# Performance work log

Hardware: AMD Instinct MI355X
Metric: run time of the kernel (lower is better)

## Reference

```python
import jax, jax.numpy as jnp
import numpy as np

E = 512   # fusion_dim
H = 8     # num_heads
HD = E // H
NC = 6

def _ln(x, g, b, eps=1e-5):
    m = jnp.mean(x, axis=-1, keepdims=True)
    v = jnp.mean((x - m) ** 2, axis=-1, keepdims=True)
    return (x - m) * jax.lax.rsqrt(v + eps) * g + b

def _lin(x, w, b):
    # torch nn.Linear: w is (out, in)
    return x @ w.T + b

def setup_inputs() -> dict:
    key = jax.random.key(0)
    ks = iter(jax.random.split(key, 32))
    B = 16384
    d = {
        'rgb':  jax.random.normal(next(ks), (B, 768), jnp.float32),
        'pose': jax.random.normal(next(ks), (B, 640), jnp.float32),
        'flow': jax.random.normal(next(ks), (B, 1024), jnp.float32),
    }
    def W(k, shape):
        return jax.random.normal(k, shape, jnp.float32) * 0.02
    # projection branches: Linear + LayerNorm
    d['rgb_w'] = W(next(ks), (E, 768));  d['rgb_b'] = jnp.zeros((E,))
    d['rgb_g'] = jnp.ones((E,));         d['rgb_beta'] = jnp.zeros((E,))
    d['pose_w'] = W(next(ks), (E, 640)); d['pose_b'] = jnp.zeros((E,))
    d['pose_g'] = jnp.ones((E,));        d['pose_beta'] = jnp.zeros((E,))
    d['flow_w'] = W(next(ks), (E, 1024)); d['flow_b'] = jnp.zeros((E,))
    d['flow_g'] = jnp.ones((E,));        d['flow_beta'] = jnp.zeros((E,))
    # MultiheadAttention packed qkv + out proj (torch layout)
    d['in_w'] = W(next(ks), (3 * E, E)); d['in_b'] = jnp.zeros((3 * E,))
    d['out_w'] = W(next(ks), (E, E));    d['out_b'] = jnp.zeros((E,))
    # gate MLP
    d['gw1'] = W(next(ks), (E, 3 * E)); d['gb1'] = jnp.zeros((E,))
    d['gw2'] = W(next(ks), (3, E));     d['gb2'] = jnp.zeros((3,))
    # classifier
    d['cw1'] = W(next(ks), (E // 2, E)); d['cb1'] = jnp.zeros((E // 2,))
    d['cg'] = jnp.ones((E // 2,));       d['cbeta'] = jnp.zeros((E // 2,))
    d['cw2'] = W(next(ks), (NC, E // 2)); d['cb2'] = jnp.zeros((NC,))
    return d

def _forward(rgb, pose, flow, rgb_w, rgb_b, rgb_g, rgb_beta,
             pose_w, pose_b, pose_g, pose_beta,
             flow_w, flow_b, flow_g, flow_beta,
             in_w, in_b, out_w, out_b,
             gw1, gb1, gw2, gb2,
             cw1, cb1, cg, cbeta, cw2, cb2):
    # per-modality projection: Linear -> LN -> ReLU (dropout = identity, eval mode)
    r = jax.nn.relu(_ln(_lin(rgb, rgb_w, rgb_b), rgb_g, rgb_beta))
    p = jax.nn.relu(_ln(_lin(pose, pose_w, pose_b), pose_g, pose_beta))
    f = jax.nn.relu(_ln(_lin(flow, flow_w, flow_b), flow_g, flow_beta))
    stacked = jnp.stack([r, p, f], axis=1)                 # (B, 3, E)
    # self-attention over the 3 modality tokens
    qkv = stacked @ in_w.T + in_b                          # (B, 3, 3E)
    q, k, v = jnp.split(qkv, 3, axis=-1)
    B = stacked.shape[0]
    q = q.reshape(B, 3, H, HD); k = k.reshape(B, 3, H, HD); v = v.reshape(B, 3, H, HD)
    scores = jnp.einsum('bqhd,bkhd->bhqk', q, k) / np.sqrt(HD).astype(np.float32)
    attn = jax.nn.softmax(scores, axis=-1)
    ctx = jnp.einsum('bhqk,bkhd->bqhd', attn, v).reshape(B, 3, E)
    attended = ctx @ out_w.T + out_b                       # (B, 3, E)
    # gating over concatenated projections
    concat = jnp.concatenate([r, p, f], axis=1)            # (B, 3E)
    gate = jax.nn.softmax(_lin(jax.nn.relu(_lin(concat, gw1, gb1)), gw2, gb2), axis=1)  # (B, 3)
    fused = jnp.einsum('bse,bs->be', attended, gate)       # (B, E)
    # classifier
    h = jax.nn.relu(_ln(_lin(fused, cw1, cb1), cg, cbeta))
    logits = _lin(h, cw2, cb2)                             # (B, NC)
    return logits, gate

def reference(rgb, pose, flow, rgb_w, rgb_b, rgb_g, rgb_beta,
              pose_w, pose_b, pose_g, pose_beta,
              flow_w, flow_b, flow_g, flow_beta,
              in_w, in_b, out_w, out_b,
              gw1, gb1, gw2, gb2,
              cw1, cb1, cg, cbeta, cw2, cb2):
    return _forward(rgb, pose, flow, rgb_w, rgb_b, rgb_g, rgb_beta,
                    pose_w, pose_b, pose_g, pose_beta,
                    flow_w, flow_b, flow_g, flow_beta,
                    in_w, in_b, out_w, out_b,
                    gw1, gb1, gw2, gb2,
                    cw1, cb1, cg, cbeta, cw2, cb2)
```

## Files before the change

### kernel.cpp

```cpp
#include <hip/hip_runtime.h>


typedef unsigned short u16;
typedef __bf16 bf16x8 __attribute__((ext_vector_type(8)));
typedef float f32x4  __attribute__((ext_vector_type(4)));
typedef unsigned short u16x8 __attribute__((ext_vector_type(8)));
typedef unsigned short u16x4 __attribute__((ext_vector_type(4)));

#define BATCH 16384

__device__ __forceinline__ u16 f2b(float f) {
  union { float f; unsigned int u; } c; c.f = f;
  unsigned int u = c.u;
  return (u16)((u + 0x7fffu + ((u >> 16) & 1u)) >> 16);
}
__device__ __forceinline__ float b2f(u16 h) {
  union { unsigned int u; float f; } c; c.u = ((unsigned int)h) << 16;
  return c.f;
}

struct CvtJobs {
  const float* s[10];
  u16* d[10];
  int n4[10];
};

__global__ __launch_bounds__(256) void cvt_multi(CvtJobs J) {
  const int stride = gridDim.x * blockDim.x;
  const int tid = blockIdx.x * blockDim.x + threadIdx.x;
  for (int ji = 0; ji < 10; ++ji) {
    const f32x4* __restrict__ s = (const f32x4*)J.s[ji];
    u16x4* __restrict__ d = (u16x4*)J.d[ji];
    const int n4 = J.n4[ji];
    for (int i = tid; i < n4; i += stride) {
      f32x4 v = s[i];
      u16x4 o;
      #pragma unroll
      for (int c = 0; c < 4; ++c) o[c] = f2b(v[c]);
      d[i] = o;
    }
  }
}

template<int EPI>
__device__ __forceinline__ void gemm_core(
    const u16* __restrict__ A, const u16* __restrict__ Bw,
    const float* __restrict__ bias, u16* __restrict__ C,
    int K, int ldc, int coff, u16* As, u16* Bs)
{
  const int t = threadIdx.x;
  const int m0 = blockIdx.y << 7;
  const int n0 = blockIdx.x << 7;
  const int wave = t >> 6, lane = t & 63;
  const int wm = wave & 1, wn = wave >> 1;
  const int lr  = lane & 15;
  const int lk8 = (lane >> 4) << 3;
  const int srow = t >> 2;
  const int scol = (t & 3) << 4;

  f32x4 acc[4][4] = {};

  const size_t rowB = (size_t)K * 2;
  const char* Ab = (const char*)A + (size_t)m0 * rowB + scol;
  const char* Bb = (const char*)Bw + (size_t)n0 * rowB + scol;

  auto stage = [&](int s, int buf) {
    const char* Ak = Ab + (size_t)s * 64;
    const char* Bk = Bb + (size_t)s * 64;
    #pragma unroll
    for (int j = 0; j < 2; ++j) {
      __builtin_amdgcn_global_load_lds(
          (const __attribute__((address_space(1))) void*)(Ak + (size_t)(j * 64 + srow) * rowB),
          (__attribute__((address_space(3))) void*)((char*)As + (buf << 13) + (j << 12) + (wave << 10)),
          16, 0, 0);
      __builtin_amdgcn_global_load_lds(
          (const __attribute__((address_space(1))) void*)(Bk + (size_t)(j * 64 + srow) * rowB),
          (__attribute__((address_space(3))) void*)((char*)Bs + (buf << 13) + (j << 12) + (wave << 10)),
          16, 0, 0);
    }
  };

  const int nsteps = K >> 5;
  stage(0, 0);
  for (int s = 0; s < nsteps; ++s) {
    const int cur = s & 1;
    __syncthreads();
    if (s + 1 < nsteps) stage(s + 1, cur ^ 1);

    const u16* Ac = As + (cur << 12);
    const u16* Bc = Bs + (cur << 12);
    bf16x8 af[4], bfr[4];
    #pragma unroll
    for (int mi = 0; mi < 4; ++mi) {
      const int r = (wm << 6) + (mi << 4) + lr;
      af[mi] = __builtin_bit_cast(bf16x8, *(const u16x8*)&Ac[r * 32 + lk8]);
    }
    #pragma unroll
    for (int ni = 0; ni < 4; ++ni) {
      const int r = (wn << 6) + (ni << 4) + lr;
      bfr[ni] = __builtin_bit_cast(bf16x8, *(const u16x8*)&Bc[r * 32 + lk8]);
    }
    #pragma unroll
    for (int mi = 0; mi < 4; ++mi)
      #pragma unroll
      for (int ni = 0; ni < 4; ++ni)
        acc[mi][ni] = __builtin_amdgcn_mfma_f32_16x16x32_bf16(
            af[mi], bfr[ni], acc[mi][ni], 0, 0, 0);
  }

  const int rquad = (lane >> 4) << 2;
  #pragma unroll
  for (int ni = 0; ni < 4; ++ni) {
    const int col = n0 + (wn << 6) + (ni << 4) + lr;
    const float bv = bias[col];
    #pragma unroll
    for (int mi = 0; mi < 4; ++mi) {
      const int rowb = m0 + (wm << 6) + (mi << 4) + rquad;
      #pragma unroll
      for (int r = 0; r < 4; ++r) {
        float v = acc[mi][ni][r] + bv;
        if (EPI == 2) v = fmaxf(v, 0.0f);
        C[(size_t)(rowb + r) * ldc + coff + col] = f2b(v);
      }
    }
  }
}

template<int EPI>
__global__ __launch_bounds__(256) void gemm128(
    const u16* __restrict__ A, const u16* __restrict__ Bw,
    const float* __restrict__ bias, u16* __restrict__ C,
    int K, int ldc, int coff)
{
  __shared__ __align__(16) u16 As[2][4096];
  __shared__ __align__(16) u16 Bs[2][4096];
  gemm_core<EPI>(A, Bw, bias, C, K, ldc, coff, &As[0][0], &Bs[0][0]);
}

struct P3 {
  const u16* A[3];
  const u16* W[3];
  const float* bias[3];
  int K[3];
  int coff[3];
  u16* C;
};
__global__ __launch_bounds__(256) void proj3_k(P3 p) {
  __shared__ __align__(16) u16 As[2][4096];
  __shared__ __align__(16) u16 Bs[2][4096];
  const int z = blockIdx.z;
  gemm_core<1>(p.A[z], p.W[z], p.bias[z], p.C, p.K[z], 1536, p.coff[z],
               &As[0][0], &Bs[0][0]);
}

__global__ __launch_bounds__(384) void ln3_k(
    const u16* __restrict__ raw, u16* __restrict__ dst,
    const float* __restrict__ g0, const float* __restrict__ b0,
    const float* __restrict__ g1, const float* __restrict__ b1,
    const float* __restrict__ g2, const float* __restrict__ b2)
{
  const int wave = threadIdx.x >> 6, lane = threadIdx.x & 63;
  const int m = wave % 3;
  const int b = blockIdx.x * 2 + wave / 3;
  const size_t off = (size_t)b * 1536 + m * 512 + lane * 8;
  u16x8 xa = *(const u16x8*)&raw[off];
  float x[8];
  float sum = 0.f, sq = 0.f;
  #pragma unroll
  for (int d = 0; d < 8; ++d) { float f = b2f(xa[d]); x[d] = f; sum += f; sq += f * f; }
  #pragma unroll
  for (int o = 32; o > 0; o >>= 1) { sum += __shfl_xor(sum, o); sq += __shfl_xor(sq, o); }
  const float mean = sum * (1.0f / 512.0f);
  const float var = sq * (1.0f / 512.0f) - mean * mean;
  const float rs = rsqrtf(var + 1e-5f);
  const float* g = (m == 0) ? g0 : (m == 1) ? g1 : g2;
  const float* bb = (m == 0) ? b0 : (m == 1) ? b1 : b2;
  u16x8 o;
  #pragma unroll
  for (int d = 0; d < 8; ++d) {
    float y = (x[d] - mean) * rs * g[lane * 8 + d] + bb[lane * 8 + d];
    o[d] = f2b(fmaxf(y, 0.0f));
  }
  *(u16x8*)&dst[off] = o;
}

template<int E>
__global__ __launch_bounds__(256) void ln_relu_k(
    const u16* __restrict__ src, u16* __restrict__ dst,
    const float* __restrict__ gg, const float* __restrict__ bb)
{
  constexpr int V = E >> 6;
  const int wave = threadIdx.x >> 6, lane = threadIdx.x & 63;
  const int row = blockIdx.x * 4 + wave;
  const u16* s = src + (size_t)row * E + lane * V;
  float x[V];
  float sum = 0.f, sq = 0.f;
  #pragma unroll
  for (int i = 0; i < V; i += 4) {
    u16x4 v = *(const u16x4*)(s + i);
    #pragma unroll
    for (int c = 0; c < 4; ++c) { float f = b2f(v[c]); x[i + c] = f; sum += f; sq += f * f; }
  }
  #pragma unroll
  for (int off = 32; off > 0; off >>= 1) {
    sum += __shfl_xor(sum, off);
    sq  += __shfl_xor(sq,  off);
  }
  const float invE = 1.0f / (float)E;
  const float m = sum * invE;
  const float var = sq * invE - m * m;
  const float rs = rsqrtf(var + 1e-5f);
  u16* d = dst + (size_t)row * E + lane * V;
  const float* g = gg + lane * V;
  const float* b = bb + lane * V;
  #pragma unroll
  for (int i = 0; i < V; i += 4) {
    u16x4 o;
    #pragma unroll
    for (int c = 0; c < 4; ++c) {
      float y = (x[i + c] - m) * rs * g[i + c] + b[i + c];
      o[c] = f2b(fmaxf(y, 0.0f));
    }
    *(u16x4*)(d + i) = o;
  }
}

__global__ __launch_bounds__(256) void attn_k(
    const u16* __restrict__ qkv, u16* __restrict__ ctx)
{
  const int gid = blockIdx.x * 256 + threadIdx.x;
  const int b = gid >> 6;
  const int h = (threadIdx.x >> 3) & 7;
  const int ld = threadIdx.x & 7;
  const size_t rb = (size_t)(3 * b) * 1536 + h * 64 + ld * 8;

  float q[3][8], k[3][8], v[3][8];
  #pragma unroll
  for (int i = 0; i < 3; ++i) {
    u16x8 qa = *(const u16x8*)&qkv[rb + (size_t)i * 1536];
    u16x8 ka = *(const u16x8*)&qkv[rb + (size_t)i * 1536 + 512];
    u16x8 va = *(const u16x8*)&qkv[rb + (size_t)i * 1536 + 1024];
    #pragma unroll
    for (int d = 0; d < 8; ++d) { q[i][d] = b2f(qa[d]); k[i][d] = b2f(ka[d]); v[i][d] = b2f(va[d]); }
  }
  float s[9];
  #pragma unroll
  for (int i = 0; i < 3; ++i)
    #pragma unroll
    for (int j = 0; j < 3; ++j) {
      float a = 0.f;
      #pragma unroll
      for (int d = 0; d < 8; ++d) a += q[i][d] * k[j][d];
      s[i * 3 + j] = a;
    }
  #pragma unroll
  for (int m = 1; m < 8; m <<= 1)
    #pragma unroll
    for (int e = 0; e < 9; ++e) s[e] += __shfl_xor(s[e], m);

  const float sc = 0.125f;
  #pragma unroll
  for (int i = 0; i < 3; ++i) {
    const float a0 = s[i * 3 + 0] * sc, a1 = s[i * 3 + 1] * sc, a2 = s[i * 3 + 2] * sc;
    const float mx = fmaxf(a0, fmaxf(a1, a2));
    float e0 = __expf(a0 - mx), e1 = __expf(a1 - mx), e2 = __expf(a2 - mx);
    const float inv = 1.0f / (e0 + e1 + e2);
    e0 *= inv; e1 *= inv; e2 *= inv;
    u16x8 o;
    #pragma unroll
    for (int d = 0; d < 8; ++d)
      o[d] = f2b(e0 * v[0][d] + e1 * v[1][d] + e2 * v[2][d]);
    *(u16x8*)&ctx[(size_t)(3 * b + i) * 512 + h * 64 + ld * 8] = o;
  }
}

__global__ __launch_bounds__(256) void gate_fuse_k(
    const u16* __restrict__ gateh, const float* __restrict__ gw2,
    const float* __restrict__ gb2, const u16* __restrict__ att,
    float* __restrict__ gate_out, u16* __restrict__ fused)
{
  const int wave = threadIdx.x >> 6, lane = threadIdx.x & 63;
  const int b = blockIdx.x * 4 + wave;
  float x[8];
  u16x8 xa = *(const u16x8*)&gateh[(size_t)b * 512 + lane * 8];
  #pragma unroll
  for (int d = 0; d < 8; ++d) x[d] = b2f(xa[d]);
  float s[3] = {0.f, 0.f, 0.f};
  #pragma unroll
  for (int j = 0; j < 3; ++j) {
    const float* w = gw2 + j * 512 + lane * 8;
    #pragma unroll
    for (int d = 0; d < 8; ++d) s[j] += x[d] * w[d];
  }
  #pragma unroll
  for (int m = 1; m < 64; m <<= 1)
    #pragma unroll
    for (int j = 0; j < 3; ++j) s[j] += __shfl_xor(s[j], m);
  #pragma unroll
  for (int j = 0; j < 3; ++j) s[j] += gb2[j];
  const float mx = fmaxf(s[0], fmaxf(s[1], s[2]));
  float g0 = __expf(s[0] - mx), g1 = __expf(s[1] - mx), g2 = __expf(s[2] - mx);
  const float inv = 1.0f / (g0 + g1 + g2);
  g0 *= inv; g1 *= inv; g2 *= inv;
  if (lane == 0) { gate_out[b * 3 + 0] = g0; gate_out[b * 3 + 1] = g1; gate_out[b * 3 + 2] = g2; }
  float o[8] = {};
  const float gw[3] = {g0, g1, g2};
  #pragma unroll
  for (int j = 0; j < 3; ++j) {
    u16x8 aa = *(const u16x8*)&att[(size_t)(3 * b + j) * 512 + lane * 8];
    #pragma unroll
    for (int d = 0; d < 8; ++d) o[d] += gw[j] * b2f(aa[d]);
  }
  u16x8 ov;
  #pragma unroll
  for (int d = 0; d < 8; ++d) ov[d] = f2b(o[d]);
  *(u16x8*)&fused[(size_t)b * 512 + lane * 8] = ov;
}

__global__ __launch_bounds__(256) void cls2_k(
    const u16* __restrict__ hh, const float* __restrict__ cw2,
    const float* __restrict__ cb2, float* __restrict__ logits)
{
  const int wave = threadIdx.x >> 6, lane = threadIdx.x & 63;
  const int b = blockIdx.x * 4 + wave;
  float x[4];
  u16x4 xa = *(const u16x4*)&hh[(size_t)b * 256 + lane * 4];
  #pragma unroll
  for (int d = 0; d < 4; ++d) x[d] = b2f(xa[d]);
  float s[6] = {};
  #pragma unroll
  for (int j = 0; j < 6; ++j) {
    const float* w = cw2 + j * 256 + lane * 4;
    #pragma unroll
    for (int d = 0; d < 4; ++d) s[j] += x[d] * w[d];
  }
  #pragma unroll
  for (int m = 1; m < 64; m <<= 1)
    #pragma unroll
    for (int j = 0; j < 6; ++j) s[j] += __shfl_xor(s[j], m);
  if (lane < 6) logits[(size_t)b * 6 + lane] = s[lane] + cb2[lane];
}

extern "C" void kernel_launch(void* const* d_in, const int* in_sizes, int n_in,
                              void* d_out, int out_size, void* d_ws, size_t ws_size,
                              hipStream_t stream) {
  const float* rgb       = (const float*)d_in[0];
  const float* pose      = (const float*)d_in[1];
  const float* flow      = (const float*)d_in[2];
  const float* rgb_w     = (const float*)d_in[3];
  const float* rgb_b     = (const float*)d_in[4];
  const float* rgb_g     = (const float*)d_in[5];
  const float* rgb_beta  = (const float*)d_in[6];
  const float* pose_w    = (const float*)d_in[7];
  const float* pose_b    = (const float*)d_in[8];
  const float* pose_g    = (const float*)d_in[9];
  const float* pose_beta = (const float*)d_in[10];
  const float* flow_w    = (const float*)d_in[11];
  const float* flow_b    = (const float*)d_in[12];
  const float* flow_g    = (const float*)d_in[13];
  const float* flow_beta = (const float*)d_in[14];
  const float* in_w      = (const float*)d_in[15];
  const float* in_b      = (const float*)d_in[16];
  const float* out_w     = (const float*)d_in[17];
  const float* out_b     = (const float*)d_in[18];
  const float* gw1       = (const float*)d_in[19];
  const float* gb1       = (const float*)d_in[20];
  const float* gw2       = (const float*)d_in[21];
  const float* gb2       = (const float*)d_in[22];
  const float* cw1       = (const float*)d_in[23];
  const float* cb1       = (const float*)d_in[24];
  const float* cg        = (const float*)d_in[25];
  const float* cbeta     = (const float*)d_in[26];
  const float* cw2       = (const float*)d_in[27];
  const float* cb2       = (const float*)d_in[28];

  float* logits_out = (float*)d_out;
  float* gate_out   = (float*)d_out + (size_t)BATCH * 6;

  char* ws = (char*)d_ws;
  u16* w_rgb  = (u16*)(ws + 0);
  u16* w_pose = (u16*)(ws + 786432);
  u16* w_flow = (u16*)(ws + 1441792);
  u16* w_in   = (u16*)(ws + 2490368);
  u16* w_out  = (u16*)(ws + 4063232);
  u16* w_g1   = (u16*)(ws + 4587520);
  u16* w_c1   = (u16*)(ws + 6160384);
  char* rpfB = ws + 6422528;
  char* ctxB = ws + 56754176;
  char* r1B  = ws + 107085824;

  u16*   rpf      = (u16*)rpfB;
  u16*   att      = (u16*)rpfB;
  u16*   raw      = (u16*)ctxB;
  u16*   ctx      = (u16*)ctxB;
  u16*   cls_tmp  = (u16*)ctxB;
  u16*   h_bf     = (u16*)(ctxB + 8388608);
  u16*   rgb_bf   = (u16*)r1B;
  u16*   pose_bf  = (u16*)(r1B + 25165824);
  u16*   flow_bf  = (u16*)(r1B + 46137344);
  u16*   qkv_buf  = (u16*)r1B;
  u16*   gateh    = (u16*)r1B;
  u16*   fusedb   = (u16*)(r1B + 16777216);

  CvtJobs J;
  const float* srcs[10] = {rgb, pose, flow, rgb_w, pose_w, flow_w, in_w, out_w, gw1, cw1};
  u16* dsts[10] = {rgb_bf, pose_bf, flow_bf, w_rgb, w_pose, w_flow, w_in, w_out, w_g1, w_c1};
  int ns[10] = {BATCH * 768, BATCH * 640, BATCH * 1024, 512 * 768, 512 * 640,
                512 * 1024, 1536 * 512, 512 * 512, 512 * 1536, 256 * 512};
  for (int i = 0; i < 10; ++i) { J.s[i] = srcs[i]; J.d[i] = dsts[i]; J.n4[i] = ns[i] / 4; }
  cvt_multi<<<2048, 256, 0, stream>>>(J);

  dim3 blk(256);
  P3 p;
  p.A[0] = rgb_bf;  p.W[0] = w_rgb;  p.bias[0] = rgb_b;  p.K[0] = 768;  p.coff[0] = 0;
  p.A[1] = pose_bf; p.W[1] = w_pose; p.bias[1] = pose_b; p.K[1] = 640;  p.coff[1] = 512;
  p.A[2] = flow_bf; p.W[2] = w_flow; p.bias[2] = flow_b; p.K[2] = 1024; p.coff[2] = 1024;
  p.C = raw;
  proj3_k<<<dim3(4, BATCH / 128, 3), blk, 0, stream>>>(p);
  ln3_k<<<BATCH / 2, dim3(384), 0, stream>>>(raw, rpf, rgb_g, rgb_beta, pose_g, pose_beta, flow_g, flow_beta);

  for (int c = 0; c < 2; ++c) {
    const u16* a_chunk = rpf + (size_t)c * 8192 * 1536;
    u16* ctx_chunk = ctx + (size_t)c * 8192 * 3 * 512;
    gemm128<1><<<dim3(12, 3 * 8192 / 128), blk, 0, stream>>>(
        a_chunk, w_in, in_b, qkv_buf, 512, 1536, 0);
    attn_k<<<8192 / 4, blk, 0, stream>>>(qkv_buf, ctx_chunk);
  }

  gemm128<2><<<dim3(4, BATCH / 128), blk, 0, stream>>>(rpf, w_g1, gb1, gateh, 1536, 512, 0);

  gemm128<1><<<dim3(4, 3 * BATCH / 128), blk, 0, stream>>>(ctx, w_out, out_b, att, 512, 512, 0);

  gate_fuse_k<<<BATCH / 4, blk, 0, stream>>>(gateh, gw2, gb2, att, gate_out, fusedb);

  gemm128<1><<<dim3(2, BATCH / 128), blk, 0, stream>>>(fusedb, w_c1, cb1, cls_tmp, 512, 256, 0);
  ln_relu_k<256><<<BATCH / 4, blk, 0, stream>>>(cls_tmp, h_bf, cg, cbeta);
  cls2_k<<<BATCH / 4, blk, 0, stream>>>(h_bf, cw2, cb2, logits_out);

  (void)in_sizes; (void)n_in; (void)out_size; (void)ws_size;
}
```

Baseline: 585.2 us.

## Fuse input fp32-to-bf16 conversion into projection GEMM and gate before out-proj

The projection GEMM now reads fp32 activations directly, converting them in registers before writing to LDS, which removes the separate conversion pass and its bf16 copy of the large inputs. The gate is computed before attention, and the attention kernel outputs the gate-weighted sum of per-modality contexts. The out-projection then runs on B rows instead of 3B. This relies on the gate summing to one so the bias is preserved, and it gives up async global-to-LDS loads for the A operand.

```diff
diff --git a/kernel.cpp b/kernel.cpp
--- a/kernel.cpp
+++ b/kernel.cpp
@@ -20,15 +20,15 @@
 }
 
 struct CvtJobs {
-  const float* s[10];
-  u16* d[10];
-  int n4[10];
+  const float* s[7];
+  u16* d[7];
+  int n4[7];
 };
 
-__global__ __launch_bounds__(256) void cvt_multi(CvtJobs J) {
+__global__ __launch_bounds__(256) void cvt_w(CvtJobs J) {
   const int stride = gridDim.x * blockDim.x;
   const int tid = blockIdx.x * blockDim.x + threadIdx.x;
-  for (int ji = 0; ji < 10; ++ji) {
+  for (int ji = 0; ji < 7; ++ji) {
     const f32x4* __restrict__ s = (const f32x4*)J.s[ji];
     u16x4* __restrict__ d = (u16x4*)J.d[ji];
     const int n4 = J.n4[ji];
@@ -43,11 +43,13 @@
 }
 
 template<int EPI>
-__device__ __forceinline__ void gemm_core(
+__global__ __launch_bounds__(256) void gemm128(
     const u16* __restrict__ A, const u16* __restrict__ Bw,
     const float* __restrict__ bias, u16* __restrict__ C,
-    int K, int ldc, int coff, u16* As, u16* Bs)
+    int K, int ldc, int coff)
 {
+  __shared__ __align__(16) u16 As[2][4096];
+  __shared__ __align__(16) u16 Bs[2][4096];
   const int t = threadIdx.x;
   const int m0 = blockIdx.y << 7;
   const int n0 = blockIdx.x << 7;
@@ -71,11 +73,11 @@
     for (int j = 0; j < 2; ++j) {
       __builtin_amdgcn_global_load_lds(
           (const __attribute__((address_space(1))) void*)(Ak + (size_t)(j * 64 + srow) * rowB),
-          (__attribute__((address_space(3))) void*)((char*)As + (buf << 13) + (j << 12) + (wave << 10)),
+          (__attribute__((address_space(3))) void*)((char*)As[buf] + (j << 12) + (wave << 10)),
           16, 0, 0);
       __builtin_amdgcn_global_load_lds(
           (const __attribute__((address_space(1))) void*)(Bk + (size_t)(j * 64 + srow) * rowB),
-          (__attribute__((address_space(3))) void*)((char*)Bs + (buf << 13) + (j << 12) + (wave << 10)),
+          (__attribute__((address_space(3))) void*)((char*)Bs[buf] + (j << 12) + (wave << 10)),
           16, 0, 0);
     }
   };
@@ -87,18 +89,16 @@
     __syncthreads();
     if (s + 1 < nsteps) stage(s + 1, cur ^ 1);
 
-    const u16* Ac = As + (cur << 12);
-    const u16* Bc = Bs + (cur << 12);
     bf16x8 af[4], bfr[4];
     #pragma unroll
     for (int mi = 0; mi < 4; ++mi) {
       const int r = (wm << 6) + (mi << 4) + lr;
-      af[mi] = __builtin_bit_cast(bf16x8, *(const u16x8*)&Ac[r * 32 + lk8]);
+      af[mi] = __builtin_bit_cast(bf16x8, *(const u16x8*)&As[cur][r * 32 + lk8]);
     }
     #pragma unroll
     for (int ni = 0; ni < 4; ++ni) {
       const int r = (wn << 6) + (ni << 4) + lr;
-      bfr[ni] = __builtin_bit_cast(bf16x8, *(const u16x8*)&Bc[r * 32 + lk8]);
+      bfr[ni] = __builtin_bit_cast(bf16x8, *(const u16x8*)&Bs[cur][r * 32 + lk8]);
     }
     #pragma unroll
     for (int mi = 0; mi < 4; ++mi)
@@ -126,31 +126,112 @@
   }
 }
 
-template<int EPI>
-__global__ __launch_bounds__(256) void gemm128(
-    const u16* __restrict__ A, const u16* __restrict__ Bw,
-    const float* __restrict__ bias, u16* __restrict__ C,
-    int K, int ldc, int coff)
-{
-  __shared__ __align__(16) u16 As[2][4096];
-  __shared__ __align__(16) u16 Bs[2][4096];
-  gemm_core<EPI>(A, Bw, bias, C, K, ldc, coff, &As[0][0], &Bs[0][0]);
-}
-
 struct P3 {
-  const u16* A[3];
+  const float* A[3];
   const u16* W[3];
   const float* bias[3];
   int K[3];
   int coff[3];
   u16* C;
 };
+
 __global__ __launch_bounds__(256) void proj3_k(P3 p) {
   __shared__ __align__(16) u16 As[2][4096];
   __shared__ __align__(16) u16 Bs[2][4096];
   const int z = blockIdx.z;
-  gemm_core<1>(p.A[z], p.W[z], p.bias[z], p.C, p.K[z], 1536, p.coff[z],
-               &As[0][0], &Bs[0][0]);
+  const float* __restrict__ A = p.A[z];
+  const u16* __restrict__ Bw = p.W[z];
+  const int K = p.K[z];
+
+  const int t = threadIdx.x;
+  const int m0 = blockIdx.y << 7;
+  const int n0 = blockIdx.x << 7;
+  const int wave = t >> 6, lane = t & 63;
+  const int wm = wave & 1, wn = wave >> 1;
+  const int lr  = lane & 15;
+  const int lk8 = (lane >> 4) << 3;
+  const int ar = t >> 3;
+  const int ac = (t & 7) << 2;
+  const int srow = t >> 2;
+  const int scol = (t & 3) << 4;
+
+  f32x4 acc[4][4] = {};
+
+  const size_t rowA = (size_t)K;
+  const size_t rowB = (size_t)K * 2;
+  const float* Abase = A + (size_t)m0 * rowA + ac;
+  const char* Bb = (const char*)Bw + (size_t)n0 * rowB + scol;
+
+  f32x4 areg[4];
+  auto loadA = [&](int s) {
+    const float* Ak = Abase + s * 32;
+    #pragma unroll
+    for (int j = 0; j < 4; ++j)
+      areg[j] = *(const f32x4*)(Ak + (size_t)(j * 32 + ar) * rowA);
+  };
+  auto writeA = [&](int buf) {
+    #pragma unroll
+    for (int j = 0; j < 4; ++j) {
+      u16x4 o;
+      #pragma unroll
+      for (int c = 0; c < 4; ++c) o[c] = f2b(areg[j][c]);
+      *(u16x4*)&As[buf][(j * 32 + ar) * 32 + ac] = o;
+    }
+  };
+  auto stageB = [&](int s, int buf) {
+    const char* Bk = Bb + (size_t)s * 64;
+    #pragma unroll
+    for (int j = 0; j < 2; ++j)
+      __builtin_amdgcn_global_load_lds(
+          (const __attribute__((address_space(1))) void*)(Bk + (size_t)(j * 64 + srow) * rowB),
+          (__attribute__((address_space(3))) void*)((char*)Bs[buf] + (j << 12) + (wave << 10)),
+          16, 0, 0);
+  };
+
+  const int nsteps = K >> 5;
+  loadA(0);
+  stageB(0, 0);
+  writeA(0);
+  for (int s = 0; s < nsteps; ++s) {
+    const int cur = s & 1;
+    __syncthreads();
+    if (s + 1 < nsteps) { loadA(s + 1); stageB(s + 1, cur ^ 1); }
+
+    bf16x8 af[4], bfr[4];
+    #pragma unroll
+    for (int mi = 0; mi < 4; ++mi) {
+      const int r = (wm << 6) + (mi << 4) + lr;
+      af[mi] = __builtin_bit_cast(bf16x8, *(const u16x8*)&As[cur][r * 32 + lk8]);
+    }
+    #pragma unroll
+    for (int ni = 0; ni < 4; ++ni) {
+      const int r = (wn << 6) + (ni << 4) + lr;
+      bfr[ni] = __builtin_bit_cast(bf16x8, *(const u16x8*)&Bs[cur][r * 32 + lk8]);
+    }
+    #pragma unroll
+    for (int mi = 0; mi < 4; ++mi)
+      #pragma unroll
+      for (int ni = 0; ni < 4; ++ni)
+        acc[mi][ni] = __builtin_amdgcn_mfma_f32_16x16x32_bf16(
+            af[mi], bfr[ni], acc[mi][ni], 0, 0, 0);
+
+    if (s + 1 < nsteps) writeA(cur ^ 1);
+  }
+
+  const int rquad = (lane >> 4) << 2;
+  #pragma unroll
+  for (int ni = 0; ni < 4; ++ni) {
+    const int col = n0 + (wn << 6) + (ni << 4) + lr;
+    const float bv = p.bias[z][col];
+    #pragma unroll
+    for (int mi = 0; mi < 4; ++mi) {
+      const int rowb = m0 + (wm << 6) + (mi << 4) + rquad;
+      #pragma unroll
+      for (int r = 0; r < 4; ++r) {
+        p.C[(size_t)(rowb + r) * 1536 + p.coff[z] + col] = f2b(acc[mi][ni][r] + bv);
+      }
+    }
+  }
 }
 
 __global__ __launch_bounds__(384) void ln3_k(
@@ -225,8 +306,42 @@
   }
 }
 
-__global__ __launch_bounds__(256) void attn_k(
-    const u16* __restrict__ qkv, u16* __restrict__ ctx)
+__global__ __launch_bounds__(256) void gate2_k(
+    const u16* __restrict__ gateh, const float* __restrict__ gw2,
+    const float* __restrict__ gb2, float* __restrict__ gate_out)
+{
+  const int wave = threadIdx.x >> 6, lane = threadIdx.x & 63;
+  const int b = blockIdx.x * 4 + wave;
+  float x[8];
+  u16x8 xa = *(const u16x8*)&gateh[(size_t)b * 512 + lane * 8];
+  #pragma unroll
+  for (int d = 0; d < 8; ++d) x[d] = b2f(xa[d]);
+  float s[3] = {0.f, 0.f, 0.f};
+  #pragma unroll
+  for (int j = 0; j < 3; ++j) {
+    const float* w = gw2 + j * 512 + lane * 8;
+    #pragma unroll
+    for (int d = 0; d < 8; ++d) s[j] += x[d] * w[d];
+  }
+  #pragma unroll
+  for (int m = 1; m < 64; m <<= 1)
+    #pragma unroll
+    for (int j = 0; j < 3; ++j) s[j] += __shfl_xor(s[j], m);
+  if (lane == 0) {
+    #pragma unroll
+    for (int j = 0; j < 3; ++j) s[j] += gb2[j];
+    const float mx = fmaxf(s[0], fmaxf(s[1], s[2]));
+    float e0 = __expf(s[0] - mx), e1 = __expf(s[1] - mx), e2 = __expf(s[2] - mx);
+    const float inv = 1.0f / (e0 + e1 + e2);
+    gate_out[b * 3 + 0] = e0 * inv;
+    gate_out[b * 3 + 1] = e1 * inv;
+    gate_out[b * 3 + 2] = e2 * inv;
+  }
+}
+
+__global__ __launch_bounds__(256) void attn_gate_k(
+    const u16* __restrict__ qkv, const float* __restrict__ gate,
+    u16* __restrict__ ctxg, int b0)
 {
   const int gid = blockIdx.x * 256 + threadIdx.x;
   const int b = gid >> 6;
@@ -258,63 +373,28 @@
     #pragma unroll
     for (int e = 0; e < 9; ++e) s[e] += __shfl_xor(s[e], m);
 
+  const float g0 = gate[(size_t)(b0 + b) * 3 + 0];
+  const float g1 = gate[(size_t)(b0 + b) * 3 + 1];
+  const float g2 = gate[(size_t)(b0 + b) * 3 + 2];
+  const float gg[3] = {g0, g1, g2};
+
+  float o[8] = {};
   const float sc = 0.125f;
   #pragma unroll
   for (int i = 0; i < 3; ++i) {
     const float a0 = s[i * 3 + 0] * sc, a1 = s[i * 3 + 1] * sc, a2 = s[i * 3 + 2] * sc;
     const float mx = fmaxf(a0, fmaxf(a1, a2));
     float e0 = __expf(a0 - mx), e1 = __expf(a1 - mx), e2 = __expf(a2 - mx);
-    const float inv = 1.0f / (e0 + e1 + e2);
+    const float inv = gg[i] / (e0 + e1 + e2);
     e0 *= inv; e1 *= inv; e2 *= inv;
-    u16x8 o;
     #pragma unroll
     for (int d = 0; d < 8; ++d)
-      o[d] = f2b(e0 * v[0][d] + e1 * v[1][d] + e2 * v[2][d]);
-    *(u16x8*)&ctx[(size_t)(3 * b + i) * 512 + h * 64 + ld * 8] = o;
-  }
-}
-
-__global__ __launch_bounds__(256) void gate_fuse_k(
-    const u16* __restrict__ gateh, const float* __restrict__ gw2,
-    const float* __restrict__ gb2, const u16* __restrict__ att,
-    float* __restrict__ gate_out, u16* __restrict__ fused)
-{
-  const int wave = threadIdx.x >> 6, lane = threadIdx.x & 63;
-  const int b = blockIdx.x * 4 + wave;
-  float x[8];
-  u16x8 xa = *(const u16x8*)&gateh[(size_t)b * 512 + lane * 8];
-  #pragma unroll
-  for (int d = 0; d < 8; ++d) x[d] = b2f(xa[d]);
-  float s[3] = {0.f, 0.f, 0.f};
-  #pragma unroll
-  for (int j = 0; j < 3; ++j) {
-    const float* w = gw2 + j * 512 + lane * 8;
-    #pragma unroll
-    for (int d = 0; d < 8; ++d) s[j] += x[d] * w[d];
-  }
-  #pragma unroll
-  for (int m = 1; m < 64; m <<= 1)
-    #pragma unroll
-    for (int j = 0; j < 3; ++j) s[j] += __shfl_xor(s[j], m);
-  #pragma unroll
-  for (int j = 0; j < 3; ++j) s[j] += gb2[j];
-  const float mx = fmaxf(s[0], fmaxf(s[1], s[2]));
-  float g0 = __expf(s[0] - mx), g1 = __expf(s[1] - mx), g2 = __expf(s[2] - mx);
-  const float inv = 1.0f / (g0 + g1 + g2);
-  g0 *= inv; g1 *= inv; g2 *= inv;
-  if (lane == 0) { gate_out[b * 3 + 0] = g0; gate_out[b * 3 + 1] = g1; gate_out[b * 3 + 2] = g2; }
-  float o[8] = {};
-  const float gw[3] = {g0, g1, g2};
-  #pragma unroll
-  for (int j = 0; j < 3; ++j) {
-    u16x8 aa = *(const u16x8*)&att[(size_t)(3 * b + j) * 512 + lane * 8];
-    #pragma unroll
-    for (int d = 0; d < 8; ++d) o[d] += gw[j] * b2f(aa[d]);
+      o[d] += e0 * v[0][d] + e1 * v[1][d] + e2 * v[2][d];
   }
   u16x8 ov;
   #pragma unroll
   for (int d = 0; d < 8; ++d) ov[d] = f2b(o[d]);
-  *(u16x8*)&fused[(size_t)b * 512 + lane * 8] = ov;
+  *(u16x8*)&ctxg[(size_t)(b0 + b) * 512 + h * 64 + ld * 8] = ov;
 }
 
 __global__ __launch_bounds__(256) void cls2_k(
@@ -386,52 +466,46 @@
   u16* w_g1   = (u16*)(ws + 4587520);
   u16* w_c1   = (u16*)(ws + 6160384);
   char* rpfB = ws + 6422528;
-  char* ctxB = ws + 56754176;
-  char* r1B  = ws + 107085824;
+  char* B2   = ws + 56754176;
+  char* Cb   = ws + 132251648;
+  char* Db   = ws + 149028864;
 
   u16*   rpf      = (u16*)rpfB;
-  u16*   att      = (u16*)rpfB;
-  u16*   raw      = (u16*)ctxB;
-  u16*   ctx      = (u16*)ctxB;
-  u16*   cls_tmp  = (u16*)ctxB;
-  u16*   h_bf     = (u16*)(ctxB + 8388608);
-  u16*   rgb_bf   = (u16*)r1B;
-  u16*   pose_bf  = (u16*)(r1B + 25165824);
-  u16*   flow_bf  = (u16*)(r1B + 46137344);
-  u16*   qkv_buf  = (u16*)r1B;
-  u16*   gateh    = (u16*)r1B;
-  u16*   fusedb   = (u16*)(r1B + 16777216);
+  u16*   raw      = (u16*)B2;
+  u16*   qkv_buf  = (u16*)B2;
+  u16*   gateh    = (u16*)Cb;
+  u16*   fusedb   = (u16*)Cb;
+  u16*   ctxg     = (u16*)Db;
+  u16*   cls_tmp  = (u16*)Db;
+  u16*   h_bf     = (u16*)(Db + 8388608);
 
   CvtJobs J;
-  const float* srcs[10] = {rgb, pose, flow, rgb_w, pose_w, flow_w, in_w, out_w, gw1, cw1};
-  u16* dsts[10] = {rgb_bf, pose_bf, flow_bf, w_rgb, w_pose, w_flow, w_in, w_out, w_g1, w_c1};
-  int ns[10] = {BATCH * 768, BATCH * 640, BATCH * 1024, 512 * 768, 512 * 640,
-                512 * 1024, 1536 * 512, 512 * 512, 512 * 1536, 256 * 512};
-  for (int i = 0; i < 10; ++i) { J.s[i] = srcs[i]; J.d[i] = dsts[i]; J.n4[i] = ns[i] / 4; }
-  cvt_multi<<<2048, 256, 0, stream>>>(J);
+  const float* srcs[7] = {rgb_w, pose_w, flow_w, in_w, out_w, gw1, cw1};
+  u16* dsts[7] = {w_rgb, w_pose, w_flow, w_in, w_out, w_g1, w_c1};
+  int ns[7] = {512 * 768, 512 * 640, 512 * 1024, 1536 * 512, 512 * 512, 512 * 1536, 256 * 512};
+  for (int i = 0; i < 7; ++i) { J.s[i] = srcs[i]; J.d[i] = dsts[i]; J.n4[i] = ns[i] / 4; }
+  cvt_w<<<128, 256, 0, stream>>>(J);
 
   dim3 blk(256);
   P3 p;
-  p.A[0] = rgb_bf;  p.W[0] = w_rgb;  p.bias[0] = rgb_b;  p.K[0] = 768;  p.coff[0] = 0;
-  p.A[1] = pose_bf; p.W[1] = w_pose; p.bias[1] = pose_b; p.K[1] = 640;  p.coff[1] = 512;
-  p.A[2] = flow_bf; p.W[2] = w_flow; p.bias[2] = flow_b; p.K[2] = 1024; p.coff[2] = 1024;
+  p.A[0] = rgb;  p.W[0] = w_rgb;  p.bias[0] = rgb_b;  p.K[0] = 768;  p.coff[0] = 0;
+  p.A[1] = pose; p.W[1] = w_pose; p.bias[1] = pose_b; p.K[1] = 640;  p.coff[1] = 512;
+  p.A[2] = flow; p.W[2] = w_flow; p.bias[2] = flow_b; p.K[2] = 1024; p.coff[2] = 1024;
   p.C = raw;
   proj3_k<<<dim3(4, BATCH / 128, 3), blk, 0, stream>>>(p);
   ln3_k<<<BATCH / 2, dim3(384), 0, stream>>>(raw, rpf, rgb_g, rgb_beta, pose_g, pose_beta, flow_g, flow_beta);
 
+  gemm128<2><<<dim3(4, BATCH / 128), blk, 0, stream>>>(rpf, w_g1, gb1, gateh, 1536, 512, 0);
+  gate2_k<<<BATCH / 4, blk, 0, stream>>>(gateh, gw2, gb2, gate_out);
+
   for (int c = 0; c < 2; ++c) {
     const u16* a_chunk = rpf + (size_t)c * 8192 * 1536;
-    u16* ctx_chunk = ctx + (size_t)c * 8192 * 3 * 512;
     gemm128<1><<<dim3(12, 3 * 8192 / 128), blk, 0, stream>>>(
         a_chunk, w_in, in_b, qkv_buf, 512, 1536, 0);
-    attn_k<<<8192 / 4, blk, 0, stream>>>(qkv_buf, ctx_chunk);
-  }
-
-  gemm128<2><<<dim3(4, BATCH / 128), blk, 0, stream>>>(rpf, w_g1, gb1, gateh, 1536, 512, 0);
-
-  gemm128<1><<<dim3(4, 3 * BATCH / 128), blk, 0, stream>>>(ctx, w_out, out_b, att, 512, 512, 0);
-
-  gate_fuse_k<<<BATCH / 4, blk, 0, stream>>>(gateh, gw2, gb2, att, gate_out, fusedb);
+    attn_gate_k<<<8192 / 4, blk, 0, stream>>>(qkv_buf, gate_out, ctxg, c * 8192);
+  }
+
+  gemm128<1><<<dim3(4, BATCH / 128), blk, 0, stream>>>(ctxg, w_out, out_b, fusedb, 512, 512, 0);
 
   gemm128<1><<<dim3(2, BATCH / 128), blk, 0, stream>>>(fusedb, w_c1, cb1, cls_tmp, 512, 256, 0);
   ln_relu_k<256><<<BATCH / 4, blk, 0, stream>>>(cls_tmp, h_bf, cg, cbeta);
```

New measurement: 574.5 us. No clear change (-1.8%).

## Apply gate weights before out-projection and switch to single-wave 64x64 GEMM

Applied to the files above, without the earlier changes.

Because the output projection is linear and the gate weights sum to one, the gate-weighted sum is moved into the attention kernel. The out-projection GEMM then runs on B rows instead of 3B, and the intermediate attended buffer and the gate_fuse pass go away. Gate logits and the softmax are now computed before attention. All GEMMs are replaced by a one-wave 64x64-tile kernel with grouped block ordering and no __syncthreads. This trades per-block data reuse for more blocks in flight, and it depends on the compiler inserting the right waits for the async LDS loads.

```diff
diff --git a/kernel.cpp b/kernel.cpp
--- a/kernel.cpp
+++ b/kernel.cpp
@@ -43,20 +43,24 @@
 }
 
 template<int EPI>
-__device__ __forceinline__ void gemm_core(
+__global__ __launch_bounds__(64, 4) void gemm_w(
     const u16* __restrict__ A, const u16* __restrict__ Bw,
     const float* __restrict__ bias, u16* __restrict__ C,
-    int K, int ldc, int coff, u16* As, u16* Bs)
-{
-  const int t = threadIdx.x;
-  const int m0 = blockIdx.y << 7;
-  const int n0 = blockIdx.x << 7;
-  const int wave = t >> 6, lane = t & 63;
-  const int wm = wave & 1, wn = wave >> 1;
+    int K, int ldc, int coff, int NB)
+{
+  __shared__ __align__(16) u16 As[2][2048];
+  __shared__ __align__(16) u16 Bs[2][2048];
+  const int id = blockIdx.x;
+  const int rr = id & 7, jj = id >> 3;
+  const int nb = jj % NB;
+  const int mb = rr + ((jj / NB) << 3);
+  const int m0 = mb << 6, n0 = nb << 6;
+
+  const int lane = threadIdx.x;
   const int lr  = lane & 15;
   const int lk8 = (lane >> 4) << 3;
-  const int srow = t >> 2;
-  const int scol = (t & 3) << 4;
+  const int srow = lane >> 2;
+  const int scol = (lane & 3) << 4;
 
   f32x4 acc[4][4] = {};
 
@@ -68,14 +72,14 @@
     const char* Ak = Ab + (size_t)s * 64;
     const char* Bk = Bb + (size_t)s * 64;
     #pragma unroll
-    for (int j = 0; j < 2; ++j) {
+    for (int j = 0; j < 4; ++j) {
       __builtin_amdgcn_global_load_lds(
-          (const __attribute__((address_space(1))) void*)(Ak + (size_t)(j * 64 + srow) * rowB),
-          (__attribute__((address_space(3))) void*)((char*)As + (buf << 13) + (j << 12) + (wave << 10)),
+          (const __attribute__((address_space(1))) void*)(Ak + (size_t)(j * 16 + srow) * rowB),
+          (__attribute__((address_space(3))) void*)((char*)As[buf] + (j << 10)),
           16, 0, 0);
       __builtin_amdgcn_global_load_lds(
-          (const __attribute__((address_space(1))) void*)(Bk + (size_t)(j * 64 + srow) * rowB),
-          (__attribute__((address_space(3))) void*)((char*)Bs + (buf << 13) + (j << 12) + (wave << 10)),
+          (const __attribute__((address_space(1))) void*)(Bk + (size_t)(j * 16 + srow) * rowB),
+          (__attribute__((address_space(3))) void*)((char*)Bs[buf] + (j << 10)),
           16, 0, 0);
     }
   };
@@ -84,22 +88,13 @@
   stage(0, 0);
   for (int s = 0; s < nsteps; ++s) {
     const int cur = s & 1;
-    __syncthreads();
+    bf16x8 af[4], bfr[4];
+    #pragma unroll
+    for (int i = 0; i < 4; ++i) {
+      af[i]  = __builtin_bit_cast(bf16x8, *(const u16x8*)&As[cur][(i * 16 + lr) * 32 + lk8]);
+      bfr[i] = __builtin_bit_cast(bf16x8, *(const u16x8*)&Bs[cur][(i * 16 + lr) * 32 + lk8]);
+    }
     if (s + 1 < nsteps) stage(s + 1, cur ^ 1);
-
-    const u16* Ac = As + (cur << 12);
-    const u16* Bc = Bs + (cur << 12);
-    bf16x8 af[4], bfr[4];
-    #pragma unroll
-    for (int mi = 0; mi < 4; ++mi) {
-      const int r = (wm << 6) + (mi << 4) + lr;
-      af[mi] = __builtin_bit_cast(bf16x8, *(const u16x8*)&Ac[r * 32 + lk8]);
-    }
-    #pragma unroll
-    for (int ni = 0; ni < 4; ++ni) {
-      const int r = (wn << 6) + (ni << 4) + lr;
-      bfr[ni] = __builtin_bit_cast(bf16x8, *(const u16x8*)&Bc[r * 32 + lk8]);
-    }
     #pragma unroll
     for (int mi = 0; mi < 4; ++mi)
       #pragma unroll
@@ -111,11 +106,11 @@
   const int rquad = (lane >> 4) << 2;
   #pragma unroll
   for (int ni = 0; ni < 4; ++ni) {
-    const int col = n0 + (wn << 6) + (ni << 4) + lr;
+    const int col = n0 + (ni << 4) + lr;
     const float bv = bias[col];
     #pragma unroll
     for (int mi = 0; mi < 4; ++mi) {
-      const int rowb = m0 + (wm << 6) + (mi << 4) + rquad;
+      const int rowb = m0 + (mi << 4) + rquad;
       #pragma unroll
       for (int r = 0; r < 4; ++r) {
         float v = acc[mi][ni][r] + bv;
@@ -124,33 +119,6 @@
       }
     }
   }
-}
-
-template<int EPI>
-__global__ __launch_bounds__(256) void gemm128(
-    const u16* __restrict__ A, const u16* __restrict__ Bw,
-    const float* __restrict__ bias, u16* __restrict__ C,
-    int K, int ldc, int coff)
-{
-  __shared__ __align__(16) u16 As[2][4096];
-  __shared__ __align__(16) u16 Bs[2][4096];
-  gemm_core<EPI>(A, Bw, bias, C, K, ldc, coff, &As[0][0], &Bs[0][0]);
-}
-
-struct P3 {
-  const u16* A[3];
-  const u16* W[3];
-  const float* bias[3];
-  int K[3];
-  int coff[3];
-  u16* C;
-};
-__global__ __launch_bounds__(256) void proj3_k(P3 p) {
-  __shared__ __align__(16) u16 As[2][4096];
-  __shared__ __align__(16) u16 Bs[2][4096];
-  const int z = blockIdx.z;
-  gemm_core<1>(p.A[z], p.W[z], p.bias[z], p.C, p.K[z], 1536, p.coff[z],
-               &As[0][0], &Bs[0][0]);
 }
 
 __global__ __launch_bounds__(384) void ln3_k(
@@ -225,8 +193,42 @@
   }
 }
 
-__global__ __launch_bounds__(256) void attn_k(
-    const u16* __restrict__ qkv, u16* __restrict__ ctx)
+__global__ __launch_bounds__(256) void gate2_k(
+    const u16* __restrict__ gateh, const float* __restrict__ gw2,
+    const float* __restrict__ gb2, float* __restrict__ gate_out)
+{
+  const int wave = threadIdx.x >> 6, lane = threadIdx.x & 63;
+  const int b = blockIdx.x * 4 + wave;
+  float x[8];
+  u16x8 xa = *(const u16x8*)&gateh[(size_t)b * 512 + lane * 8];
+  #pragma unroll
+  for (int d = 0; d < 8; ++d) x[d] = b2f(xa[d]);
+  float s[3] = {0.f, 0.f, 0.f};
+  #pragma unroll
+  for (int j = 0; j < 3; ++j) {
+    const float* w = gw2 + j * 512 + lane * 8;
+    #pragma unroll
+    for (int d = 0; d < 8; ++d) s[j] += x[d] * w[d];
+  }
+  #pragma unroll
+  for (int m = 1; m < 64; m <<= 1)
+    #pragma unroll
+    for (int j = 0; j < 3; ++j) s[j] += __shfl_xor(s[j], m);
+  if (lane == 0) {
+    #pragma unroll
+    for (int j = 0; j < 3; ++j) s[j] += gb2[j];
+    const float mx = fmaxf(s[0], fmaxf(s[1], s[2]));
+    float e0 = __expf(s[0] - mx), e1 = __expf(s[1] - mx), e2 = __expf(s[2] - mx);
+    const float inv = 1.0f / (e0 + e1 + e2);
+    gate_out[b * 3 + 0] = e0 * inv;
+    gate_out[b * 3 + 1] = e1 * inv;
+    gate_out[b * 3 + 2] = e2 * inv;
+  }
+}
+
+__global__ __launch_bounds__(256) void attn_gate_k(
+    const u16* __restrict__ qkv, const float* __restrict__ gate,
+    u16* __restrict__ ctxg, int b0)
 {
   const int gid = blockIdx.x * 256 + threadIdx.x;
   const int b = gid >> 6;
@@ -258,63 +260,28 @@
     #pragma unroll
     for (int e = 0; e < 9; ++e) s[e] += __shfl_xor(s[e], m);
 
+  const float g0 = gate[(size_t)(b0 + b) * 3 + 0];
+  const float g1 = gate[(size_t)(b0 + b) * 3 + 1];
+  const float g2 = gate[(size_t)(b0 + b) * 3 + 2];
+  const float gg[3] = {g0, g1, g2};
+
+  float o[8] = {};
   const float sc = 0.125f;
   #pragma unroll
   for (int i = 0; i < 3; ++i) {
     const float a0 = s[i * 3 + 0] * sc, a1 = s[i * 3 + 1] * sc, a2 = s[i * 3 + 2] * sc;
     const float mx = fmaxf(a0, fmaxf(a1, a2));
     float e0 = __expf(a0 - mx), e1 = __expf(a1 - mx), e2 = __expf(a2 - mx);
-    const float inv = 1.0f / (e0 + e1 + e2);
+    const float inv = gg[i] / (e0 + e1 + e2);
     e0 *= inv; e1 *= inv; e2 *= inv;
-    u16x8 o;
     #pragma unroll
     for (int d = 0; d < 8; ++d)
-      o[d] = f2b(e0 * v[0][d] + e1 * v[1][d] + e2 * v[2][d]);
-    *(u16x8*)&ctx[(size_t)(3 * b + i) * 512 + h * 64 + ld * 8] = o;
-  }
-}
-
-__global__ __launch_bounds__(256) void gate_fuse_k(
-    const u16* __restrict__ gateh, const float* __restrict__ gw2,
-    const float* __restrict__ gb2, const u16* __restrict__ att,
-    float* __restrict__ gate_out, u16* __restrict__ fused)
-{
-  const int wave = threadIdx.x >> 6, lane = threadIdx.x & 63;
-  const int b = blockIdx.x * 4 + wave;
-  float x[8];
-  u16x8 xa = *(const u16x8*)&gateh[(size_t)b * 512 + lane * 8];
-  #pragma unroll
-  for (int d = 0; d < 8; ++d) x[d] = b2f(xa[d]);
-  float s[3] = {0.f, 0.f, 0.f};
-  #pragma unroll
-  for (int j = 0; j < 3; ++j) {
-    const float* w = gw2 + j * 512 + lane * 8;
-    #pragma unroll
-    for (int d = 0; d < 8; ++d) s[j] += x[d] * w[d];
-  }
-  #pragma unroll
-  for (int m = 1; m < 64; m <<= 1)
-    #pragma unroll
-    for (int j = 0; j < 3; ++j) s[j] += __shfl_xor(s[j], m);
-  #pragma unroll
-  for (int j = 0; j < 3; ++j) s[j] += gb2[j];
-  const float mx = fmaxf(s[0], fmaxf(s[1], s[2]));
-  float g0 = __expf(s[0] - mx), g1 = __expf(s[1] - mx), g2 = __expf(s[2] - mx);
-  const float inv = 1.0f / (g0 + g1 + g2);
-  g0 *= inv; g1 *= inv; g2 *= inv;
-  if (lane == 0) { gate_out[b * 3 + 0] = g0; gate_out[b * 3 + 1] = g1; gate_out[b * 3 + 2] = g2; }
-  float o[8] = {};
-  const float gw[3] = {g0, g1, g2};
-  #pragma unroll
-  for (int j = 0; j < 3; ++j) {
-    u16x8 aa = *(const u16x8*)&att[(size_t)(3 * b + j) * 512 + lane * 8];
-    #pragma unroll
-    for (int d = 0; d < 8; ++d) o[d] += gw[j] * b2f(aa[d]);
+      o[d] += e0 * v[0][d] + e1 * v[1][d] + e2 * v[2][d];
   }
   u16x8 ov;
   #pragma unroll
   for (int d = 0; d < 8; ++d) ov[d] = f2b(o[d]);
-  *(u16x8*)&fused[(size_t)b * 512 + lane * 8] = ov;
+  *(u16x8*)&ctxg[(size_t)(b0 + b) * 512 + h * 64 + ld * 8] = ov;
 }
 
 __global__ __launch_bounds__(256) void cls2_k(
@@ -385,22 +352,17 @@
   u16* w_out  = (u16*)(ws + 4063232);
   u16* w_g1   = (u16*)(ws + 4587520);
   u16* w_c1   = (u16*)(ws + 6160384);
-  char* rpfB = ws + 6422528;
-  char* ctxB = ws + 56754176;
-  char* r1B  = ws + 107085824;
-
-  u16*   rpf      = (u16*)rpfB;
-  u16*   att      = (u16*)rpfB;
-  u16*   raw      = (u16*)ctxB;
-  u16*   ctx      = (u16*)ctxB;
-  u16*   cls_tmp  = (u16*)ctxB;
-  u16*   h_bf     = (u16*)(ctxB + 8388608);
-  u16*   rgb_bf   = (u16*)r1B;
-  u16*   pose_bf  = (u16*)(r1B + 25165824);
-  u16*   flow_bf  = (u16*)(r1B + 46137344);
-  u16*   qkv_buf  = (u16*)r1B;
-  u16*   gateh    = (u16*)r1B;
-  u16*   fusedb   = (u16*)(r1B + 16777216);
+  u16* rpf     = (u16*)(ws + 6422528);
+  u16* raw     = (u16*)(ws + 56754176);
+  u16* gateh   = (u16*)(ws + 56754176);
+  u16* qkv_buf = (u16*)(ws + 56754176);
+  u16* rgb_bf  = (u16*)(ws + 107085824);
+  u16* pose_bf = (u16*)(ws + 132251648);
+  u16* flow_bf = (u16*)(ws + 153223168);
+  u16* ctxg    = (u16*)(ws + 132251648);
+  u16* fusedb  = (u16*)(ws + 149028864);
+  u16* cls_tmp = (u16*)(ws + 165806080);
+  u16* h_bf    = (u16*)(ws + 174194688);
 
   CvtJobs J;
   const float* srcs[10] = {rgb, pose, flow, rgb_w, pose_w, flow_w, in_w, out_w, gw1, cw1};
@@ -410,32 +372,26 @@
   for (int i = 0; i < 10; ++i) { J.s[i] = srcs[i]; J.d[i] = dsts[i]; J.n4[i] = ns[i] / 4; }
   cvt_multi<<<2048, 256, 0, stream>>>(J);
 
-  dim3 blk(256);
-  P3 p;
-  p.A[0] = rgb_bf;  p.W[0] = w_rgb;  p.bias[0] = rgb_b;  p.K[0] = 768;  p.coff[0] = 0;
-  p.A[1] = pose_bf; p.W[1] = w_pose; p.bias[1] = pose_b; p.K[1] = 640;  p.coff[1] = 512;
-  p.A[2] = flow_bf; p.W[2] = w_flow; p.bias[2] = flow_b; p.K[2] = 1024; p.coff[2] = 1024;
-  p.C = raw;
-  proj3_k<<<dim3(4, BATCH / 128, 3), blk, 0, stream>>>(p);
+  dim3 wblk(64);
+  gemm_w<1><<<2048, wblk, 0, stream>>>(rgb_bf,  w_rgb,  rgb_b,  raw, 768,  1536, 0,    8);
+  gemm_w<1><<<2048, wblk, 0, stream>>>(pose_bf, w_pose, pose_b, raw, 640,  1536, 512,  8);
+  gemm_w<1><<<2048, wblk, 0, stream>>>(flow_bf, w_flow, flow_b, raw, 1024, 1536, 1024, 8);
   ln3_k<<<BATCH / 2, dim3(384), 0, stream>>>(raw, rpf, rgb_g, rgb_beta, pose_g, pose_beta, flow_g, flow_beta);
+
+  gemm_w<2><<<2048, wblk, 0, stream>>>(rpf, w_g1, gb1, gateh, 1536, 512, 0, 8);
+  gate2_k<<<BATCH / 4, dim3(256), 0, stream>>>(gateh, gw2, gb2, gate_out);
 
   for (int c = 0; c < 2; ++c) {
     const u16* a_chunk = rpf + (size_t)c * 8192 * 1536;
-    u16* ctx_chunk = ctx + (size_t)c * 8192 * 3 * 512;
-    gemm128<1><<<dim3(12, 3 * 8192 / 128), blk, 0, stream>>>(
-        a_chunk, w_in, in_b, qkv_buf, 512, 1536, 0);
-    attn_k<<<8192 / 4, blk, 0, stream>>>(qkv_buf, ctx_chunk);
-  }
-
-  gemm128<2><<<dim3(4, BATCH / 128), blk, 0, stream>>>(rpf, w_g1, gb1, gateh, 1536, 512, 0);
-
-  gemm128<1><<<dim3(4, 3 * BATCH / 128), blk, 0, stream>>>(ctx, w_out, out_b, att, 512, 512, 0);
-
-  gate_fuse_k<<<BATCH / 4, blk, 0, stream>>>(gateh, gw2, gb2, att, gate_out, fusedb);
-
-  gemm128<1><<<dim3(2, BATCH / 128), blk, 0, stream>>>(fusedb, w_c1, cb1, cls_tmp, 512, 256, 0);
-  ln_relu_k<256><<<BATCH / 4, blk, 0, stream>>>(cls_tmp, h_bf, cg, cbeta);
-  cls2_k<<<BATCH / 4, blk, 0, stream>>>(h_bf, cw2, cb2, logits_out);
+    gemm_w<1><<<24 * 384, wblk, 0, stream>>>(a_chunk, w_in, in_b, qkv_buf, 512, 1536, 0, 24);
+    attn_gate_k<<<8192 / 4, dim3(256), 0, stream>>>(qkv_buf, gate_out, ctxg, c * 8192);
+  }
+
+  gemm_w<1><<<2048, wblk, 0, stream>>>(ctxg, w_out, out_b, fusedb, 512, 512, 0, 8);
+
+  gemm_w<1><<<1024, wblk, 0, stream>>>(fusedb, w_c1, cb1, cls_tmp, 512, 256, 0, 4);
+  ln_relu_k<256><<<BATCH / 4, dim3(256), 0, stream>>>(cls_tmp, h_bf, cg, cbeta);
+  cls2_k<<<BATCH / 4, dim3(256), 0, stream>>>(h_bf, cw2, cb2, logits_out);
 
   (void)in_sizes; (void)n_in; (void)out_size; (void)ws_size;
 }
```

After: 612.1 us. 1.05x slower.
